# Optimization experiments

Measured on AMD Instinct MI355X. Metric: run time of the kernel, lower is better.

The kernel has to match this reference:

```python
import jax, jax.numpy as jnp
import numpy as np

INF, OUTF, BIT, GROUPSIZE = 4096, 11008, 4, 128
GROUPS = INF // GROUPSIZE  # 32
PACK = 32 // BIT           # 8 values per int32


def setup_inputs() -> dict:
    key = jax.random.key(0)
    k1, k2, k3, k4, k5 = jax.random.split(key, 5)
    x = jax.random.normal(k1, (2, 2048, INF), dtype=jnp.float32)
    # packed 4-bit weights: (INF*BIT/32, OUTF) int32
    qweight = jax.random.randint(k2, (INF * BIT // 32, OUTF), 0, 2147483647, dtype=jnp.int32)
    scales = jax.random.uniform(k3, (OUTF, GROUPS, 1), dtype=jnp.float32) * 0.01 + 0.001
    zeros = jax.random.uniform(k4, (OUTF, GROUPS, 1), dtype=jnp.float32) * 0.1
    bias = jax.random.normal(k5, (OUTF,), dtype=jnp.float32)
    return {"x": x, "qweight": qweight, "scales": scales, "zeros": zeros, "bias": bias}


def _dequant(qweight, scales, zeros):
    # unpack 8 nibbles per int32 row -> intweight (INF, OUTF)
    shifts = (BIT * jnp.arange(PACK, dtype=jnp.int32))[None, :, None]  # (1,8,1)
    nibbles = (qweight[:, None, :] >> shifts) & 0xF                    # (INF/8, 8, OUTF)
    wq = nibbles.reshape(INF, OUTF).astype(jnp.float32)
    # per-group dequant: W[k,n] = q*scale[n, k//gs] - zero[n, k//gs]
    s = scales[:, :, 0].T[:, None, :]  # (GROUPS, 1, OUTF)
    z = zeros[:, :, 0].T[:, None, :]
    w = wq.reshape(GROUPS, GROUPSIZE, OUTF) * s - z
    return w.reshape(INF, OUTF)


def reference(x, qweight, scales, zeros, bias):
    w = _dequant(qweight, scales, zeros)  # (INF, OUTF)
    # y = x @ W + bias  (matches y init to bias then vecquant4matmul accumulate)
    return jnp.einsum('bsk,kn->bsn', x, w) + bias
```

## Files before the change

kernel.cpp:

```cpp
#include <hip/hip_runtime.h>
#include <hip/hip_bf16.h>
#include <cstdint>
#include <cstddef>

#define K_DIM   4096
#define N_DIM   11008
#define M_DIM   4096
#define GROUPS  32
#define QROWS   512

typedef __bf16 bf16x8 __attribute__((ext_vector_type(8)));
typedef float  f32x4  __attribute__((ext_vector_type(4)));

__device__ __forceinline__ void async16(const void* g, void* lds) {
    __builtin_amdgcn_global_load_lds(
        (const __attribute__((address_space(1))) uint32_t*)g,
        (__attribute__((address_space(3))) uint32_t*)lds,
        16, 0, 0);
}

#define FENCE() asm volatile("" ::: "memory")
#define BAR()   do { FENCE(); __builtin_amdgcn_s_barrier(); FENCE(); } while (0)

#define DQ_NN   64
#define DQ_KK   32
#define DQ_ROW  264
__global__ __launch_bounds__(256) void dequant_kernel(
        const uint32_t* __restrict__ qw,
        const float* __restrict__ scales,
        const float* __restrict__ zeros,
        __bf16* __restrict__ Wt) {
    __shared__ __align__(16) __bf16 T[DQ_NN * DQ_ROW];

    const int n0  = blockIdx.x * DQ_NN;
    const int kk0 = blockIdx.y * DQ_KK;
    const int tid = threadIdx.x;

#pragma unroll
    for (int it = 0; it < 8; ++it) {
        const int flat = it * 256 + tid;
        const int kk_l = flat >> 6;
        const int n_l  = flat & 63;
        const int kk   = kk0 + kk_l;
        const int n    = n0 + n_l;
        const uint32_t q = qw[(size_t)kk * N_DIM + n];
        const int g = kk >> 4;
        const float s = scales[(size_t)n * GROUPS + g];
        const float z = zeros[(size_t)n * GROUPS + g];
        bf16x8 w;
#pragma unroll
        for (int j = 0; j < 8; ++j) {
            float v = (float)((q >> (4 * j)) & 0xF) * s - z;
            w[j] = (__bf16)v;
        }
        *(bf16x8*)(&T[n_l * DQ_ROW + kk_l * 8]) = w;
    }
    __syncthreads();

#pragma unroll
    for (int it = 0; it < 8; ++it) {
        const int flat = it * 256 + tid;
        const int n_l    = flat >> 5;
        const int kchunk = flat & 31;
        bf16x8 v = *(const bf16x8*)(&T[n_l * DQ_ROW + kchunk * 8]);
        *(bf16x8*)(Wt + (size_t)(n0 + n_l) * K_DIM + (size_t)kk0 * 8 + kchunk * 8) = v;
    }
}

__global__ __launch_bounds__(256) void xconv_kernel(
        const float* __restrict__ x, __bf16* __restrict__ xb) {
    const size_t i = ((size_t)blockIdx.x * 256 + threadIdx.x) * 8;
    const float4* p = (const float4*)(x + i);
    float4 a = p[0];
    float4 b = p[1];
    bf16x8 o;
    o[0] = (__bf16)a.x; o[1] = (__bf16)a.y; o[2] = (__bf16)a.z; o[3] = (__bf16)a.w;
    o[4] = (__bf16)b.x; o[5] = (__bf16)b.y; o[6] = (__bf16)b.z; o[7] = (__bf16)b.w;
    *(bf16x8*)(xb + i) = o;
}

#define BM 256
#define BN 256
#define BK 64
#define NT 43
#define MT 16
#define NWG (NT*MT)

#define MFMA4(AV, R)                                                          \
    acc[(R)][0] = __builtin_amdgcn_mfma_f32_16x16x32_bf16((AV), b0, acc[(R)][0], 0,0,0); \
    acc[(R)][1] = __builtin_amdgcn_mfma_f32_16x16x32_bf16((AV), b1, acc[(R)][1], 0,0,0); \
    acc[(R)][2] = __builtin_amdgcn_mfma_f32_16x16x32_bf16((AV), b2, acc[(R)][2], 0,0,0); \
    acc[(R)][3] = __builtin_amdgcn_mfma_f32_16x16x32_bf16((AV), b3, acc[(R)][3], 0,0,0);

template<bool DO_STAGE>
__device__ __forceinline__ void kgroup(
        const __bf16* __restrict__ ar0, const __bf16* __restrict__ ar1,
        const __bf16* __restrict__ br0, const __bf16* __restrict__ br1,
        const __bf16* (&gsrc)[8], __bf16* lds, const int (&ldst)[8],
        const int soff, f32x4 (&acc)[8][4])
{
    bf16x8 a0, a1, a2, a3, b0, b1, b2, b3;

    asm volatile("s_waitcnt vmcnt(0)" ::: "memory");
    BAR();

    if constexpr (DO_STAGE) {
        async16(gsrc[0], lds + ldst[0] + soff);
        async16(gsrc[1], lds + ldst[1] + soff);
        async16(gsrc[2], lds + ldst[2] + soff);
        async16(gsrc[3], lds + ldst[3] + soff);
    }
    a0 = *(const bf16x8*)(ar0 + 0*1024);
    a1 = *(const bf16x8*)(ar0 + 1*1024);
    a2 = *(const bf16x8*)(ar0 + 2*1024);
    a3 = *(const bf16x8*)(ar0 + 3*1024);
    b0 = *(const bf16x8*)(br0 + 0*1024);
    b1 = *(const bf16x8*)(br0 + 1*1024);
    b2 = *(const bf16x8*)(br0 + 2*1024);
    b3 = *(const bf16x8*)(br0 + 3*1024);
    __builtin_amdgcn_s_setprio(1);
    MFMA4(a0, 0) MFMA4(a1, 1) MFMA4(a2, 2) MFMA4(a3, 3)
    __builtin_amdgcn_s_setprio(0);

    if constexpr (DO_STAGE) {
        async16(gsrc[4], lds + ldst[4] + soff);
        async16(gsrc[5], lds + ldst[5] + soff);
        async16(gsrc[6], lds + ldst[6] + soff);
        async16(gsrc[7], lds + ldst[7] + soff);
    }
    a0 = *(const bf16x8*)(ar0 + 4*1024);
    a1 = *(const bf16x8*)(ar0 + 5*1024);
    a2 = *(const bf16x8*)(ar0 + 6*1024);
    a3 = *(const bf16x8*)(ar0 + 7*1024);
    __builtin_amdgcn_s_setprio(1);
    MFMA4(a0, 4) MFMA4(a1, 5) MFMA4(a2, 6) MFMA4(a3, 7)
    __builtin_amdgcn_s_setprio(0);

    a0 = *(const bf16x8*)(ar1 + 0*1024);
    a1 = *(const bf16x8*)(ar1 + 1*1024);
    a2 = *(const bf16x8*)(ar1 + 2*1024);
    a3 = *(const bf16x8*)(ar1 + 3*1024);
    b0 = *(const bf16x8*)(br1 + 0*1024);
    b1 = *(const bf16x8*)(br1 + 1*1024);
    b2 = *(const bf16x8*)(br1 + 2*1024);
    b3 = *(const bf16x8*)(br1 + 3*1024);
    __builtin_amdgcn_s_setprio(1);
    MFMA4(a0, 0) MFMA4(a1, 1) MFMA4(a2, 2) MFMA4(a3, 3)
    __builtin_amdgcn_s_setprio(0);

    a0 = *(const bf16x8*)(ar1 + 4*1024);
    a1 = *(const bf16x8*)(ar1 + 5*1024);
    a2 = *(const bf16x8*)(ar1 + 6*1024);
    a3 = *(const bf16x8*)(ar1 + 7*1024);
    __builtin_amdgcn_s_setprio(1);
    MFMA4(a0, 4) MFMA4(a1, 5) MFMA4(a2, 6) MFMA4(a3, 7)
    __builtin_amdgcn_s_setprio(0);

    if constexpr (DO_STAGE) {
#pragma unroll
        for (int j = 0; j < 8; ++j) gsrc[j] += BK;
    }
}

__global__ __launch_bounds__(512, 2) void gemm_kernel(
        const __bf16* __restrict__ A,
        const __bf16* __restrict__ Bt,
        const float* __restrict__ bias,
        float* __restrict__ C) {
    __shared__ __align__(16) __bf16 lds[65536];

    const int tid  = threadIdx.x;
    const int wave = tid >> 6;
    const int lane = tid & 63;
    const int wm   = wave >> 2;
    const int wn   = wave & 3;
    const int quad = lane >> 4;
    const int l16  = lane & 15;

    const int bid = blockIdx.x;
    const int swz = (bid & 7) * (NWG / 8) + (bid >> 3);
    const int n_t = swz >> 4;
    const int m_t = swz & 15;
    const int m0 = m_t << 8;
    const int n0 = n_t << 8;

    f32x4 acc[8][4] = {};

    const int srow = tid >> 3;
    const int scol = ((tid & 7) ^ (srow & 7)) << 3;

    const __bf16* gsrc[8];
    gsrc[0] = A  + (size_t)(m0 +   0 + srow) * K_DIM + scol;
    gsrc[1] = A  + (size_t)(m0 + 128 + srow) * K_DIM + scol;
    gsrc[2] = Bt + (size_t)(n0 +   0 + srow) * K_DIM + scol;
    gsrc[3] = Bt + (size_t)(n0 +  64 + srow) * K_DIM + scol;
    gsrc[4] = Bt + (size_t)(n0 + 128 + srow) * K_DIM + scol;
    gsrc[5] = Bt + (size_t)(n0 + 192 + srow) * K_DIM + scol;
    gsrc[6] = A  + (size_t)(m0 +  64 + srow) * K_DIM + scol;
    gsrc[7] = A  + (size_t)(m0 + 192 + srow) * K_DIM + scol;

    const int wq = wave << 9;
    const int ldst[8] = {
        0*4096 + wq,          2*4096 + wq,
        32768 + 0*4096 + wq,  32768 + 1*4096 + wq,
        32768 + 2*4096 + wq,  32768 + 3*4096 + wq,
        1*4096 + wq,          3*4096 + wq
    };

#pragma unroll
    for (int j = 0; j < 8; ++j) async16(gsrc[j], lds + ldst[j]);
#pragma unroll
    for (int j = 0; j < 8; ++j) gsrc[j] += BK;

    const int h3  = l16 & 7;
    const int cc0 = (quad ^ h3) << 3;
    const int cc1 = ((quad ^ h3) ^ 4) << 3;
    const int arow = (wm << 7) + l16;
    const int brow = (wn << 6) + l16;

    const __bf16* a00 = lds + arow * 64 + cc0;
    const __bf16* a01 = lds + arow * 64 + cc1;
    const __bf16* b00 = lds + 32768 + brow * 64 + cc0;
    const __bf16* b01 = lds + 32768 + brow * 64 + cc1;

#pragma unroll 1
    for (int gg = 0; gg < 31; ++gg) {
        kgroup<true>(a00,         a01,         b00,         b01,
                     gsrc, lds, ldst, 16384, acc);
        kgroup<true>(a00 + 16384, a01 + 16384, b00 + 16384, b01 + 16384,
                     gsrc, lds, ldst, 0,     acc);
    }
    kgroup<true >(a00,         a01,         b00,         b01,
                  gsrc, lds, ldst, 16384, acc);
    kgroup<false>(a00 + 16384, a01 + 16384, b00 + 16384, b01 + 16384,
                  gsrc, lds, ldst, 0,     acc);

#pragma unroll
    for (int nf = 0; nf < 4; ++nf) {
        const int n = n0 + (wn << 6) + (nf << 4) + l16;
        const float bv = bias[n];
#pragma unroll
        for (int mf = 0; mf < 8; ++mf) {
            const int mrow = m0 + (wm << 7) + (mf << 4) + (quad << 2);
            float* cp = C + (size_t)mrow * N_DIM + n;
#pragma unroll
            for (int r = 0; r < 4; ++r)
                cp[(size_t)r * N_DIM] = acc[mf][nf][r] + bv;
        }
    }
}

extern "C" void kernel_launch(void* const* d_in, const int* in_sizes, int n_in,
                              void* d_out, int out_size, void* d_ws, size_t ws_size,
                              hipStream_t stream) {
    const float*    x      = (const float*)d_in[0];
    const uint32_t* qw     = (const uint32_t*)d_in[1];
    const float*    scales = (const float*)d_in[2];
    const float*    zeros  = (const float*)d_in[3];
    const float*    bias   = (const float*)d_in[4];
    float*          out    = (float*)d_out;

    __bf16* Wt = (__bf16*)d_ws;
    __bf16* xb = (__bf16*)((char*)d_ws + (size_t)N_DIM * K_DIM * sizeof(__bf16));

    dim3 dq_grid(N_DIM / DQ_NN, QROWS / DQ_KK);
    dequant_kernel<<<dq_grid, 256, 0, stream>>>(qw, scales, zeros, Wt);
    xconv_kernel<<<(M_DIM * K_DIM) / (256 * 8), 256, 0, stream>>>(x, xb);

    gemm_kernel<<<NWG, 512, 0, stream>>>(xb, Wt, bias, out);
}
```

Baseline: 595.9 us.

## Fuse 4-bit weight dequantization into GEMM main loop, drop separate dequant kernel

Removes the standalone dequant kernel that wrote a full bf16 transposed weight matrix to global memory. The GEMM instead loads packed int4 words plus transposed scale/zero values in registers, dequantizes them, and writes swizzled bf16 tiles into LDS each k-step. A small kernel transposes scales/zeros into a group-major interleaved layout. This avoids the weight write and re-read traffic and one launch. In exchange it adds ALU work and synchronous LDS writes inside the MFMA loop, plus an extra lgkmcnt wait. Each of the 16 M-tiles repeats dequantization of the same weights.

```diff
diff --git a/kernel.cpp b/kernel.cpp
--- a/kernel.cpp
+++ b/kernel.cpp
@@ -22,49 +22,14 @@
 #define FENCE() asm volatile("" ::: "memory")
 #define BAR()   do { FENCE(); __builtin_amdgcn_s_barrier(); FENCE(); } while (0)
 
-#define DQ_NN   64
-#define DQ_KK   32
-#define DQ_ROW  264
-__global__ __launch_bounds__(256) void dequant_kernel(
-        const uint32_t* __restrict__ qw,
-        const float* __restrict__ scales,
-        const float* __restrict__ zeros,
-        __bf16* __restrict__ Wt) {
-    __shared__ __align__(16) __bf16 T[DQ_NN * DQ_ROW];
-
-    const int n0  = blockIdx.x * DQ_NN;
-    const int kk0 = blockIdx.y * DQ_KK;
-    const int tid = threadIdx.x;
-
-#pragma unroll
-    for (int it = 0; it < 8; ++it) {
-        const int flat = it * 256 + tid;
-        const int kk_l = flat >> 6;
-        const int n_l  = flat & 63;
-        const int kk   = kk0 + kk_l;
-        const int n    = n0 + n_l;
-        const uint32_t q = qw[(size_t)kk * N_DIM + n];
-        const int g = kk >> 4;
-        const float s = scales[(size_t)n * GROUPS + g];
-        const float z = zeros[(size_t)n * GROUPS + g];
-        bf16x8 w;
-#pragma unroll
-        for (int j = 0; j < 8; ++j) {
-            float v = (float)((q >> (4 * j)) & 0xF) * s - z;
-            w[j] = (__bf16)v;
-        }
-        *(bf16x8*)(&T[n_l * DQ_ROW + kk_l * 8]) = w;
-    }
-    __syncthreads();
-
-#pragma unroll
-    for (int it = 0; it < 8; ++it) {
-        const int flat = it * 256 + tid;
-        const int n_l    = flat >> 5;
-        const int kchunk = flat & 31;
-        bf16x8 v = *(const bf16x8*)(&T[n_l * DQ_ROW + kchunk * 8]);
-        *(bf16x8*)(Wt + (size_t)(n0 + n_l) * K_DIM + (size_t)kk0 * 8 + kchunk * 8) = v;
-    }
+__global__ __launch_bounds__(256) void szt_kernel(
+        const float* __restrict__ s, const float* __restrict__ z,
+        float* __restrict__ szT) {
+    const int n = blockIdx.x * 256 + threadIdx.x;
+    const int g = blockIdx.y;
+    const size_t o = ((size_t)g * (N_DIM / 4) + (n >> 2)) * 8 + (n & 3);
+    szT[o]     = s[(size_t)n * GROUPS + g];
+    szT[o + 4] = z[(size_t)n * GROUPS + g];
 }
 
 __global__ __launch_bounds__(256) void xconv_kernel(
@@ -92,23 +57,51 @@
     acc[(R)][2] = __builtin_amdgcn_mfma_f32_16x16x32_bf16((AV), b2, acc[(R)][2], 0,0,0); \
     acc[(R)][3] = __builtin_amdgcn_mfma_f32_16x16x32_bf16((AV), b3, acc[(R)][3], 0,0,0);
 
-template<bool DO_STAGE>
+#define DQ_WRITE(QV, SV, ZV, SOFF)                                            \
+    do {                                                                      \
+        const uint32_t qa_[4] = { (QV).x, (QV).y, (QV).z, (QV).w };           \
+        const float    sa_[4] = { (SV).x, (SV).y, (SV).z, (SV).w };           \
+        const float    za_[4] = { (ZV).x, (ZV).y, (ZV).z, (ZV).w };           \
+        _Pragma("unroll")                                                     \
+        for (int j = 0; j < 4; ++j) {                                         \
+            const uint32_t qv = qa_[j];                                       \
+            const float sj = sa_[j], zj = za_[j];                             \
+            bf16x8 w;                                                         \
+            _Pragma("unroll")                                                 \
+            for (int i = 0; i < 8; ++i)                                       \
+                w[i] = (__bf16)((float)((qv >> (4 * i)) & 0xFu) * sj - zj);   \
+            const int r_ = (ng << 2) + j;                                     \
+            *(bf16x8*)(lds + 32768 + (SOFF) + r_ * 64 +                       \
+                       ((kkl ^ (r_ & 7)) << 3)) = w;                          \
+        }                                                                     \
+    } while (0)
+
+template<bool STAGE, bool ADV>
 __device__ __forceinline__ void kgroup(
         const __bf16* __restrict__ ar0, const __bf16* __restrict__ ar1,
         const __bf16* __restrict__ br0, const __bf16* __restrict__ br1,
-        const __bf16* (&gsrc)[8], __bf16* lds, const int (&ldst)[8],
+        const __bf16* (&gsrcA)[4], __bf16* lds, const int (&ldstA)[4],
+        const uint32_t*& qwp, const float*& szp,
         const int soff, f32x4 (&acc)[8][4])
 {
+    const int tid = threadIdx.x;
+    const int kkl = tid & 7;
+    const int ng  = tid >> 3;
     bf16x8 a0, a1, a2, a3, b0, b1, b2, b3;
-
+    uint4 qf; float4 sf, zf;
+
+    asm volatile("s_waitcnt lgkmcnt(0)" ::: "memory");
     asm volatile("s_waitcnt vmcnt(0)" ::: "memory");
     BAR();
 
-    if constexpr (DO_STAGE) {
-        async16(gsrc[0], lds + ldst[0] + soff);
-        async16(gsrc[1], lds + ldst[1] + soff);
-        async16(gsrc[2], lds + ldst[2] + soff);
-        async16(gsrc[3], lds + ldst[3] + soff);
+    if constexpr (STAGE) {
+        async16(gsrcA[0], lds + ldstA[0] + soff);
+        async16(gsrcA[1], lds + ldstA[1] + soff);
+        async16(gsrcA[2], lds + ldstA[2] + soff);
+        async16(gsrcA[3], lds + ldstA[3] + soff);
+        qf = *(const uint4*)qwp;
+        sf = *(const float4*)szp;
+        zf = *(const float4*)(szp + 4);
     }
     a0 = *(const bf16x8*)(ar0 + 0*1024);
     a1 = *(const bf16x8*)(ar0 + 1*1024);
@@ -122,12 +115,6 @@
     MFMA4(a0, 0) MFMA4(a1, 1) MFMA4(a2, 2) MFMA4(a3, 3)
     __builtin_amdgcn_s_setprio(0);
 
-    if constexpr (DO_STAGE) {
-        async16(gsrc[4], lds + ldst[4] + soff);
-        async16(gsrc[5], lds + ldst[5] + soff);
-        async16(gsrc[6], lds + ldst[6] + soff);
-        async16(gsrc[7], lds + ldst[7] + soff);
-    }
     a0 = *(const bf16x8*)(ar0 + 4*1024);
     a1 = *(const bf16x8*)(ar0 + 5*1024);
     a2 = *(const bf16x8*)(ar0 + 6*1024);
@@ -144,6 +131,9 @@
     b1 = *(const bf16x8*)(br1 + 1*1024);
     b2 = *(const bf16x8*)(br1 + 2*1024);
     b3 = *(const bf16x8*)(br1 + 3*1024);
+    if constexpr (STAGE) {
+        DQ_WRITE(qf, sf, zf, soff);
+    }
     __builtin_amdgcn_s_setprio(1);
     MFMA4(a0, 0) MFMA4(a1, 1) MFMA4(a2, 2) MFMA4(a3, 3)
     __builtin_amdgcn_s_setprio(0);
@@ -156,15 +146,18 @@
     MFMA4(a0, 4) MFMA4(a1, 5) MFMA4(a2, 6) MFMA4(a3, 7)
     __builtin_amdgcn_s_setprio(0);
 
-    if constexpr (DO_STAGE) {
-#pragma unroll
-        for (int j = 0; j < 8; ++j) gsrc[j] += BK;
+    if constexpr (STAGE) {
+#pragma unroll
+        for (int j = 0; j < 4; ++j) gsrcA[j] += BK;
+        qwp += 8 * N_DIM;
+        if constexpr (ADV) szp += 2 * N_DIM;
     }
 }
 
 __global__ __launch_bounds__(512, 2) void gemm_kernel(
         const __bf16* __restrict__ A,
-        const __bf16* __restrict__ Bt,
+        const uint32_t* __restrict__ qw,
+        const float* __restrict__ szT,
         const float* __restrict__ bias,
         float* __restrict__ C) {
     __shared__ __align__(16) __bf16 lds[65536];
@@ -189,28 +182,30 @@
     const int srow = tid >> 3;
     const int scol = ((tid & 7) ^ (srow & 7)) << 3;
 
-    const __bf16* gsrc[8];
-    gsrc[0] = A  + (size_t)(m0 +   0 + srow) * K_DIM + scol;
-    gsrc[1] = A  + (size_t)(m0 + 128 + srow) * K_DIM + scol;
-    gsrc[2] = Bt + (size_t)(n0 +   0 + srow) * K_DIM + scol;
-    gsrc[3] = Bt + (size_t)(n0 +  64 + srow) * K_DIM + scol;
-    gsrc[4] = Bt + (size_t)(n0 + 128 + srow) * K_DIM + scol;
-    gsrc[5] = Bt + (size_t)(n0 + 192 + srow) * K_DIM + scol;
-    gsrc[6] = A  + (size_t)(m0 +  64 + srow) * K_DIM + scol;
-    gsrc[7] = A  + (size_t)(m0 + 192 + srow) * K_DIM + scol;
+    const __bf16* gsrcA[4];
+#pragma unroll
+    for (int q = 0; q < 4; ++q)
+        gsrcA[q] = A + (size_t)(m0 + q * 64 + srow) * K_DIM + scol;
 
     const int wq = wave << 9;
-    const int ldst[8] = {
-        0*4096 + wq,          2*4096 + wq,
-        32768 + 0*4096 + wq,  32768 + 1*4096 + wq,
-        32768 + 2*4096 + wq,  32768 + 3*4096 + wq,
-        1*4096 + wq,          3*4096 + wq
-    };
-
-#pragma unroll
-    for (int j = 0; j < 8; ++j) async16(gsrc[j], lds + ldst[j]);
-#pragma unroll
-    for (int j = 0; j < 8; ++j) gsrc[j] += BK;
+    const int ldstA[4] = { 0*4096 + wq, 1*4096 + wq, 2*4096 + wq, 3*4096 + wq };
+
+    const int kkl = tid & 7;
+    const int ng  = tid >> 3;
+    const uint32_t* qwp = qw + (size_t)kkl * N_DIM + n0 + (ng << 2);
+    const float*    szp = szT + ((size_t)(n0 >> 2) + ng) * 8;
+
+#pragma unroll
+    for (int q = 0; q < 4; ++q) async16(gsrcA[q], lds + ldstA[q]);
+#pragma unroll
+    for (int q = 0; q < 4; ++q) gsrcA[q] += BK;
+    {
+        uint4 q0 = *(const uint4*)qwp;
+        float4 s0 = *(const float4*)szp;
+        float4 z0 = *(const float4*)(szp + 4);
+        qwp += 8 * N_DIM;
+        DQ_WRITE(q0, s0, z0, 0);
+    }
 
     const int h3  = l16 & 7;
     const int cc0 = (quad ^ h3) << 3;
@@ -225,15 +220,15 @@
 
 #pragma unroll 1
     for (int gg = 0; gg < 31; ++gg) {
-        kgroup<true>(a00,         a01,         b00,         b01,
-                     gsrc, lds, ldst, 16384, acc);
-        kgroup<true>(a00 + 16384, a01 + 16384, b00 + 16384, b01 + 16384,
-                     gsrc, lds, ldst, 0,     acc);
-    }
-    kgroup<true >(a00,         a01,         b00,         b01,
-                  gsrc, lds, ldst, 16384, acc);
-    kgroup<false>(a00 + 16384, a01 + 16384, b00 + 16384, b01 + 16384,
-                  gsrc, lds, ldst, 0,     acc);
+        kgroup<true, true >(a00,         a01,         b00,         b01,
+                            gsrcA, lds, ldstA, qwp, szp, 16384, acc);
+        kgroup<true, false>(a00 + 16384, a01 + 16384, b00 + 16384, b01 + 16384,
+                            gsrcA, lds, ldstA, qwp, szp, 0,     acc);
+    }
+    kgroup<true,  false>(a00,         a01,         b00,         b01,
+                         gsrcA, lds, ldstA, qwp, szp, 16384, acc);
+    kgroup<false, false>(a00 + 16384, a01 + 16384, b00 + 16384, b01 + 16384,
+                         gsrcA, lds, ldstA, qwp, szp, 0,     acc);
 
 #pragma unroll
     for (int nf = 0; nf < 4; ++nf) {
@@ -254,18 +249,16 @@
                               void* d_out, int out_size, void* d_ws, size_t ws_size,
                               hipStream_t stream) {
     const float*    x      = (const float*)d_in[0];
-    const uint32_t* qw     = (const uint32_t*)d_in[1];
+    const uint32_t* qwv    = (const uint32_t*)d_in[1];
     const float*    scales = (const float*)d_in[2];
     const float*    zeros  = (const float*)d_in[3];
     const float*    bias   = (const float*)d_in[4];
     float*          out    = (float*)d_out;
 
-    __bf16* Wt = (__bf16*)d_ws;
-    __bf16* xb = (__bf16*)((char*)d_ws + (size_t)N_DIM * K_DIM * sizeof(__bf16));
-
-    dim3 dq_grid(N_DIM / DQ_NN, QROWS / DQ_KK);
-    dequant_kernel<<<dq_grid, 256, 0, stream>>>(qw, scales, zeros, Wt);
+    __bf16* xb  = (__bf16*)d_ws;
+    float*  szT = (float*)((char*)d_ws + (size_t)M_DIM * K_DIM * sizeof(__bf16));
+
+    szt_kernel<<<dim3(N_DIM / 256, GROUPS), 256, 0, stream>>>(scales, zeros, szT);
     xconv_kernel<<<(M_DIM * K_DIM) / (256 * 8), 256, 0, stream>>>(x, xb);
-
-    gemm_kernel<<<NWG, 512, 0, stream>>>(xb, Wt, bias, out);
-}
+    gemm_kernel<<<NWG, 512, 0, stream>>>(xb, qwv, szT, bias, out);
+}
```

Result: slower. 650.2 us (+9.1%).
